# Kernel tuning notes

Measured on AMD Instinct MI355X. Metric: run time of the kernel, lower is better.

Reference implementation:

```python
import jax, jax.numpy as jnp
import numpy as np

B, N, L, OUT = 64, 100, 32, 3
EDGE_SIZES = [64, 64]   # edge MLP widths per mp step
NODE_SIZES = [64, 32]   # node MLP widths per mp step
ALPHA = 0.1             # leaky relu slope
NUM_MPS = 2
EPS = 1e-12             # for differentiable euclidean norm


def _lin_init(key, fan_in, fan_out):
    k1, k2 = jax.random.split(key)
    s = 1.0 / np.sqrt(fan_in)
    w = jax.random.uniform(k1, (fan_in, fan_out), jnp.float32, -s, s)
    b = jax.random.uniform(k2, (fan_out,), jnp.float32, -s, s)
    return w, b


def setup_inputs() -> dict:
    key = jax.random.key(0)
    ks = iter(jax.random.split(key, 32))
    inp = {"x": jax.random.normal(next(ks), (B, L), jnp.float32)}
    # global latent map: Linear(L, N*L)
    inp["lin_w"], inp["lin_b"] = _lin_init(next(ks), L, N * L)
    d = L
    for i in range(NUM_MPS):
        e_in = 2 * d + 1  # [x_i, x_j, dist_ij]
        inp[f"e{i}_w0"], inp[f"e{i}_b0"] = _lin_init(next(ks), e_in, EDGE_SIZES[0])
        inp[f"e{i}_w1"], inp[f"e{i}_b1"] = _lin_init(next(ks), EDGE_SIZES[0], EDGE_SIZES[1])
        n_in = d + EDGE_SIZES[1]  # [x, aggregated edges]
        inp[f"n{i}_w0"], inp[f"n{i}_b0"] = _lin_init(next(ks), n_in, NODE_SIZES[0])
        inp[f"n{i}_w1"], inp[f"n{i}_b1"] = _lin_init(next(ks), NODE_SIZES[0], NODE_SIZES[1])
        d = NODE_SIZES[1]
    inp["out_w"], inp["out_b"] = _lin_init(next(ks), d, OUT)
    return inp


def _mlp(h, layers, alpha):
    for w, b in layers:
        h = jax.nn.leaky_relu(h @ w + b, alpha)
    return h


def _forward(x, lin_w, lin_b,
             e0_w0, e0_b0, e0_w1, e0_b1, n0_w0, n0_b0, n0_w1, n0_b1,
             e1_w0, e1_b0, e1_w1, e1_b1, n1_w0, n1_b0, n1_w1, n1_b1,
             out_w, out_b):
    # latent map: [B, L] -> [B, N, L]
    h = (x @ lin_w + lin_b).reshape(-1, N, L)
    steps = [
        ([(e0_w0, e0_b0), (e0_w1, e0_b1)], [(n0_w0, n0_b0), (n0_w1, n0_b1)]),
        ([(e1_w0, e1_b0), (e1_w1, e1_b1)], [(n1_w0, n1_b0), (n1_w1, n1_b1)]),
    ]
    for edge_layers, node_layers in steps:
        b, n, d = h.shape
        xi = h[:, :, None, :]  # [B, N, 1, d] (receiver)
        xj = h[:, None, :, :]  # [B, 1, N, d] (sender)
        # euclidean pairwise distance, eps for differentiability at 0
        dist = jnp.sqrt(jnp.sum((xi - xj) ** 2, axis=-1, keepdims=True) + EPS)
        e_in = jnp.concatenate([
            jnp.broadcast_to(xi, (b, n, n, d)),
            jnp.broadcast_to(xj, (b, n, n, d)),
            dist,
        ], axis=-1)                       # [B, N, N, 2d+1]
        A = _mlp(e_in, edge_layers, ALPHA)  # [B, N, N, e_out]
        agg = A.sum(axis=2)               # sum over senders -> [B, N, e_out]
        h = _mlp(jnp.concatenate([h, agg], axis=-1), node_layers, ALPHA)
    out = h @ out_w + out_b               # [B, N, OUT]
    return jnp.tanh(out)                  # normalize_output=True


def reference(x, lin_w, lin_b,
              e0_w0, e0_b0, e0_w1, e0_b1, n0_w0, n0_b0, n0_w1, n0_b1,
              e1_w0, e1_b0, e1_w1, e1_b1, n1_w0, n1_b0, n1_w1, n1_b1,
              out_w, out_b):
    return _forward(x, lin_w, lin_b,
                    e0_w0, e0_b0, e0_w1, e0_b1, n0_w0, n0_b0, n0_w1, n0_b1,
                    e1_w0, e1_b0, e1_w1, e1_b1, n1_w0, n1_b0, n1_w1, n1_b1,
                    out_w, out_b)
```

## Files before the change

kernel.cpp:

```cpp
#include <hip/hip_runtime.h>

#define NB 64
#define NN 100
#define DL 32
#define BN (NB * NN)

typedef _Float16 f16x8 __attribute__((ext_vector_type(8)));
typedef float f32x4 __attribute__((ext_vector_type(4)));

static __device__ __forceinline__ float lrelu(float x) { return fmaxf(x, 0.1f * x); }
static __device__ __forceinline__ f32x4 ld4(const float* p) { return *(const f32x4*)p; }
static __device__ __forceinline__ float hsum4(f32x4 v) { return v[0] + v[1] + v[2] + v[3]; }

__global__ __launch_bounds__(256) void k_pre(
    const float* __restrict__ x, const float* __restrict__ lw, const float* __restrict__ lb,
    const float* __restrict__ ew0, const float* __restrict__ eb0,
    const float* __restrict__ w1a, const float* __restrict__ w1b,
    float* __restrict__ h, float* __restrict__ U, _Float16* __restrict__ V,
    _Float16* __restrict__ PW) {
    int blk = blockIdx.x;
    int t = threadIdx.x;
    if (blk >= 1600) {
        int step = blk - 1600;
        const float* w1 = step ? w1b : w1a;
        _Float16* dst = PW + step * 4096;
#pragma unroll
        for (int u = 0; u < 16; ++u) {
            int idx = t * 16 + u;
            int jj = idx & 7, lane = (idx >> 3) & 63, hf = (idx >> 9) & 1, kt = idx >> 10;
            int c = hf * 32 + (lane >> 4) * 8 + jj;
            int k = kt * 16 + (lane & 15);
            dst[idx] = (_Float16)w1[c * 64 + k];
        }
        return;
    }
    __shared__ float xs[DL];
    __shared__ float hs[4][DL];
    int row0 = blk * 4;
    int b = row0 / NN;
    if (t < DL) xs[t] = x[b * DL + t];
    __syncthreads();
    if (t < 128) {
        int ni = t >> 5, c = t & 31;
        int n = (row0 + ni) % NN;
        float s = lb[n * DL + c];
#pragma unroll
        for (int cc = 0; cc < DL; ++cc) s += xs[cc] * lw[cc * 3200 + n * DL + c];
        hs[ni][c] = s;
        h[(row0 + ni) * DL + c] = s;
    }
    __syncthreads();
#pragma unroll
    for (int r = 0; r < 2; ++r) {
        int o = r * 256 + t;
        int ni = o >> 7, kw = o & 127;
        int which = kw >> 6, k = kw & 63;
        const float* wp = ew0 + (which ? DL * 64 : 0) + k;
        float s = which ? 0.f : eb0[k];
#pragma unroll
        for (int c = 0; c < DL; ++c) s += hs[ni][c] * wp[c * 64];
        if (which) V[(row0 + ni) * 64 + k] = (_Float16)s;
        else       U[(row0 + ni) * 64 + k] = s;
    }
}

template <int FINAL>
__global__ __launch_bounds__(256) void k_edge(
    const float* __restrict__ h, const float* __restrict__ U, const _Float16* __restrict__ V,
    const float* __restrict__ w0, const _Float16* __restrict__ PW,
    const float* __restrict__ b1,
    const float* __restrict__ w0n, const float* __restrict__ b0n,
    const float* __restrict__ w1n, const float* __restrict__ b1n,
    const float* __restrict__ wA, const float* __restrict__ bA,
    float* __restrict__ hout, float* __restrict__ Uo, _Float16* __restrict__ Vo,
    float* __restrict__ out) {
    __shared__ __align__(16) _Float16 pwl[4096];
    __shared__ float sdist[4][112];
    __shared__ __align__(16) float sxin[4][96];
    __shared__ __align__(16) float st0[4][64];
    __shared__ __align__(16) float sh2[4][32];

    int t = threadIdx.x;
    {
        const f16x8* srcp = (const f16x8*)PW;
        f16x8* dstp = (f16x8*)pwl;
        dstp[t] = srcp[t];
        dstp[t + 256] = srcp[t + 256];
    }
    int w = t >> 6, lane = t & 63, q = lane >> 4, kk = lane & 15;
    int bi = blockIdx.x * 4 + w;
    int b = bi / NN;

    if (lane < 32) sxin[w][lane] = h[bi * DL + lane];

    {
        int g = lane >> 3, r = lane & 7;
        f32x4 hi4 = ld4(h + bi * DL + r * 4);
        const float* hb = h + b * NN * DL;
#pragma unroll
        for (int it = 0; it < 14; ++it) {
            int j = it * 8 + g;
            int jc = j < NN ? j : NN - 1;
            f32x4 hj4 = ld4(hb + jc * DL + r * 4);
            f32x4 dd = hi4 - hj4;
            float s = dd[0] * dd[0] + dd[1] * dd[1] + dd[2] * dd[2] + dd[3] * dd[3];
            s += __shfl_xor(s, 1);
            s += __shfl_xor(s, 2);
            s += __shfl_xor(s, 4);
            if (r == 0) sdist[w][j] = sqrtf(s + 1e-12f);
        }
    }

    int c0 = q * 8;
    f16x8 ulo, uhi, wdlo, wdhi;
    {
        const float* Up = U + (size_t)bi * 64;
        f32x4 a0 = ld4(Up + c0), a1 = ld4(Up + c0 + 4);
        f32x4 a2 = ld4(Up + 32 + c0), a3 = ld4(Up + 36 + c0);
        const float* wd = w0 + 64 * 64;
        f32x4 d0 = ld4(wd + c0), d1 = ld4(wd + c0 + 4);
        f32x4 d2 = ld4(wd + 32 + c0), d3 = ld4(wd + 36 + c0);
#pragma unroll
        for (int i = 0; i < 4; ++i) {
            ulo[i] = (_Float16)a0[i];  ulo[i + 4] = (_Float16)a1[i];
            uhi[i] = (_Float16)a2[i];  uhi[i + 4] = (_Float16)a3[i];
            wdlo[i] = (_Float16)d0[i]; wdlo[i + 4] = (_Float16)d1[i];
            wdhi[i] = (_Float16)d2[i]; wdhi[i + 4] = (_Float16)d3[i];
        }
    }
    float b1k[4];
#pragma unroll
    for (int kt = 0; kt < 4; ++kt) b1k[kt] = b1[kt * 16 + kk];
    float m6 = (q == 0) ? 1.f : 0.f;

    const _Float16* Vb = V + (size_t)b * NN * 64;
    f16x8 vlo, vhi;
    {
        const _Float16* vr = Vb + kk * 64 + c0;
        vlo = *(const f16x8*)vr;
        vhi = *(const f16x8*)(vr + 32);
    }

    __syncthreads();
    float dj = sdist[w][kk];

    float sacc[4] = {0.f, 0.f, 0.f, 0.f};
    unsigned pb = 0;
#pragma unroll
    for (int jt = 0; jt < 7; ++jt) {
        _Float16 djh = (_Float16)dj;
        f16x8 dj8;
#pragma unroll
        for (int i = 0; i < 8; ++i) dj8[i] = djh;
        f16x8 A0 = __builtin_elementwise_fma(dj8, wdlo, ulo + vlo);
        f16x8 A1 = __builtin_elementwise_fma(dj8, wdhi, uhi + vhi);
        A0 = __builtin_elementwise_max(A0, (_Float16)0.1f * A0);
        A1 = __builtin_elementwise_max(A1, (_Float16)0.1f * A1);

        if (jt < 6) {
            int j = (jt + 1) * 16 + kk;
            int jc = (jt == 5 && j >= NN) ? NN - 1 : j;
            const _Float16* vr = Vb + jc * 64 + c0;
            vlo = *(const f16x8*)vr;
            vhi = *(const f16x8*)(vr + 32);
            dj = sdist[w][j];
        }
        asm volatile("" : "+v"(pb));
        const _Float16* pB = (const _Float16*)((const char*)pwl + pb);
#pragma unroll
        for (int kt = 0; kt < 4; ++kt) {
            f16x8 B0 = *(const f16x8*)&pB[(kt * 2 + 0) * 512 + lane * 8];
            f16x8 B1 = *(const f16x8*)&pB[(kt * 2 + 1) * 512 + lane * 8];
            f32x4 a = {0.f, 0.f, 0.f, 0.f};
            a = __builtin_amdgcn_mfma_f32_16x16x32_f16(A0, B0, a, 0, 0, 0);
            a = __builtin_amdgcn_mfma_f32_16x16x32_f16(A1, B1, a, 0, 0, 0);
            f32x4 s4 = a + b1k[kt];
            s4 = __builtin_elementwise_max(s4, 0.1f * s4);
            float hs = hsum4(s4);
            sacc[kt] += (jt == 6) ? hs * m6 : hs;
        }
    }

    {
        float ag[4];
#pragma unroll
        for (int kt = 0; kt < 4; ++kt) {
            float s = sacc[kt];
            s += __shfl_xor(s, 16);
            s += __shfl_xor(s, 32);
            ag[kt] = s;
        }
        if (lane < 16) {
#pragma unroll
            for (int kt = 0; kt < 4; ++kt) sxin[w][32 + kt * 16 + lane] = ag[kt];
        }
    }

    {
        float sa = 0.f, sb = 0.f, sc = 0.f, sd = 0.f;
#pragma unroll
        for (int c = 0; c < 96; c += 4) {
            sa += sxin[w][c + 0] * w0n[(c + 0) * 64 + lane];
            sb += sxin[w][c + 1] * w0n[(c + 1) * 64 + lane];
            sc += sxin[w][c + 2] * w0n[(c + 2) * 64 + lane];
            sd += sxin[w][c + 3] * w0n[(c + 3) * 64 + lane];
        }
        st0[w][lane] = lrelu((sa + sb) + (sc + sd) + b0n[lane]);
    }
    {
        int k2 = lane & 31, p = lane >> 5;
        float sa = 0.f, sb = 0.f;
#pragma unroll
        for (int cc = 0; cc < 32; cc += 2) {
            int c = p * 32 + cc;
            sa += st0[w][c] * w1n[c * DL + k2];
            sb += st0[w][c + 1] * w1n[(c + 1) * DL + k2];
        }
        float s = sa + sb;
        s += __shfl_xor(s, 32);
        if (lane < 32) {
            float hv = lrelu(s + b1n[lane]);
            sh2[w][lane] = hv;
            if (!FINAL) hout[bi * DL + lane] = hv;
        }
    }

    if (FINAL) {
        if (lane < 3) {
            float s = bA[lane];
#pragma unroll
            for (int c = 0; c < DL; ++c) s += sh2[w][c] * wA[c * 3 + lane];
            out[bi * 3 + lane] = tanhf(s);
        }
    } else {
        float su = bA[lane], sv = 0.f;
#pragma unroll
        for (int c = 0; c < DL; ++c) {
            float hv = sh2[w][c];
            su += hv * wA[c * 64 + lane];
            sv += hv * wA[(DL + c) * 64 + lane];
        }
        Uo[bi * 64 + lane] = su;
        Vo[bi * 64 + lane] = (_Float16)sv;
    }
}

extern "C" void kernel_launch(void* const* d_in, const int* in_sizes, int n_in,
                              void* d_out, int out_size, void* d_ws, size_t ws_size,
                              hipStream_t stream) {
    const float* x     = (const float*)d_in[0];
    const float* lin_w = (const float*)d_in[1];
    const float* lin_b = (const float*)d_in[2];
    const float* ew0[2] = {(const float*)d_in[3],  (const float*)d_in[11]};
    const float* eb0[2] = {(const float*)d_in[4],  (const float*)d_in[12]};
    const float* ew1[2] = {(const float*)d_in[5],  (const float*)d_in[13]};
    const float* eb1[2] = {(const float*)d_in[6],  (const float*)d_in[14]};
    const float* nw0[2] = {(const float*)d_in[7],  (const float*)d_in[15]};
    const float* nb0[2] = {(const float*)d_in[8],  (const float*)d_in[16]};
    const float* nw1[2] = {(const float*)d_in[9],  (const float*)d_in[17]};
    const float* nb1[2] = {(const float*)d_in[10], (const float*)d_in[18]};
    const float* ow = (const float*)d_in[19];
    const float* ob = (const float*)d_in[20];
    float* out = (float*)d_out;

    float* h    = (float*)d_ws;
    float* h2   = h + 204800;
    float* U    = h2 + 204800;
    float* U2   = U + 409600;
    _Float16* V  = (_Float16*)(U2 + 409600);
    _Float16* V2 = V + 409600;
    _Float16* PW = V2 + 409600;

    k_pre<<<1602, 256, 0, stream>>>(x, lin_w, lin_b, ew0[0], eb0[0], ew1[0], ew1[1],
                                    h, U, V, PW);
    k_edge<0><<<1600, 256, 0, stream>>>(h, U, V, ew0[0], PW, eb1[0],
                                        nw0[0], nb0[0], nw1[0], nb1[0],
                                        ew0[1], eb0[1], h2, U2, V2, nullptr);
    k_edge<1><<<1600, 256, 0, stream>>>(h2, U2, V2, ew0[1], PW + 4096, eb1[1],
                                        nw0[1], nb0[1], nw1[1], nb1[1],
                                        ow, ob, nullptr, nullptr, nullptr, out);
}
```

Measured before the change: 174.1 us.

## Split each node's sender tiles across two waves per block

Each block now processes one receiver node with two waves that split the seven sender tiles, combining partial aggregates via shared memory. The node MLP and next-step U/V projections are also split between the two waves. This shortens the per-wave serial chain and raises parallelism. In exchange it adds block barriers and copies the shared edge weight tile into LDS once per node instead of once per four nodes.

```diff
diff --git a/kernel.cpp b/kernel.cpp
--- a/kernel.cpp
+++ b/kernel.cpp
@@ -65,7 +65,7 @@
 }
 
 template <int FINAL>
-__global__ __launch_bounds__(256) void k_edge(
+__global__ __launch_bounds__(128) void k_edge(
     const float* __restrict__ h, const float* __restrict__ U, const _Float16* __restrict__ V,
     const float* __restrict__ w0, const _Float16* __restrict__ PW,
     const float* __restrict__ b1,
@@ -75,31 +75,36 @@
     float* __restrict__ hout, float* __restrict__ Uo, _Float16* __restrict__ Vo,
     float* __restrict__ out) {
     __shared__ __align__(16) _Float16 pwl[4096];
-    __shared__ float sdist[4][112];
-    __shared__ __align__(16) float sxin[4][96];
-    __shared__ __align__(16) float st0[4][64];
-    __shared__ __align__(16) float sh2[4][32];
+    __shared__ float sdist[112];
+    __shared__ __align__(16) float sxin[32];
+    __shared__ __align__(16) float aggp[2][64];
+    __shared__ __align__(16) float red[2][64];
+    __shared__ __align__(16) float st0[64];
+    __shared__ __align__(16) float sh2[32];
 
     int t = threadIdx.x;
     {
         const f16x8* srcp = (const f16x8*)PW;
         f16x8* dstp = (f16x8*)pwl;
         dstp[t] = srcp[t];
+        dstp[t + 128] = srcp[t + 128];
         dstp[t + 256] = srcp[t + 256];
+        dstp[t + 384] = srcp[t + 384];
     }
     int w = t >> 6, lane = t & 63, q = lane >> 4, kk = lane & 15;
-    int bi = blockIdx.x * 4 + w;
+    int bi = blockIdx.x;
     int b = bi / NN;
 
-    if (lane < 32) sxin[w][lane] = h[bi * DL + lane];
+    if (t < 32) sxin[t] = h[bi * DL + t];
 
     {
         int g = lane >> 3, r = lane & 7;
+        int jbase = w * 48;
         f32x4 hi4 = ld4(h + bi * DL + r * 4);
         const float* hb = h + b * NN * DL;
 #pragma unroll
-        for (int it = 0; it < 14; ++it) {
-            int j = it * 8 + g;
+        for (int it = 0; it < 8; ++it) {
+            int j = jbase + it * 8 + g;
             int jc = j < NN ? j : NN - 1;
             f32x4 hj4 = ld4(hb + jc * DL + r * 4);
             f32x4 dd = hi4 - hj4;
@@ -107,7 +112,7 @@
             s += __shfl_xor(s, 1);
             s += __shfl_xor(s, 2);
             s += __shfl_xor(s, 4);
-            if (r == 0) sdist[w][j] = sqrtf(s + 1e-12f);
+            if (r == 0) sdist[j] = sqrtf(s + 1e-12f);
         }
     }
 
@@ -134,20 +139,21 @@
     float m6 = (q == 0) ? 1.f : 0.f;
 
     const _Float16* Vb = V + (size_t)b * NN * 64;
+    int jt0 = w ? 3 : 0;
     f16x8 vlo, vhi;
     {
-        const _Float16* vr = Vb + kk * 64 + c0;
+        const _Float16* vr = Vb + (jt0 * 16 + kk) * 64 + c0;
         vlo = *(const f16x8*)vr;
         vhi = *(const f16x8*)(vr + 32);
     }
 
     __syncthreads();
-    float dj = sdist[w][kk];
+    float dj = sdist[jt0 * 16 + kk];
 
     float sacc[4] = {0.f, 0.f, 0.f, 0.f};
     unsigned pb = 0;
-#pragma unroll
-    for (int jt = 0; jt < 7; ++jt) {
+
+    auto tile = [&](int jt, int last, int pf) {
         _Float16 djh = (_Float16)dj;
         f16x8 dj8;
 #pragma unroll
@@ -156,14 +162,13 @@
         f16x8 A1 = __builtin_elementwise_fma(dj8, wdhi, uhi + vhi);
         A0 = __builtin_elementwise_max(A0, (_Float16)0.1f * A0);
         A1 = __builtin_elementwise_max(A1, (_Float16)0.1f * A1);
-
-        if (jt < 6) {
+        if (pf) {
             int j = (jt + 1) * 16 + kk;
-            int jc = (jt == 5 && j >= NN) ? NN - 1 : j;
+            int jc = j < NN ? j : NN - 1;
             const _Float16* vr = Vb + jc * 64 + c0;
             vlo = *(const f16x8*)vr;
             vhi = *(const f16x8*)(vr + 32);
-            dj = sdist[w][j];
+            dj = sdist[j];
         }
         asm volatile("" : "+v"(pb));
         const _Float16* pB = (const _Float16*)((const char*)pwl + pb);
@@ -177,71 +182,70 @@
             f32x4 s4 = a + b1k[kt];
             s4 = __builtin_elementwise_max(s4, 0.1f * s4);
             float hs = hsum4(s4);
-            sacc[kt] += (jt == 6) ? hs * m6 : hs;
-        }
-    }
-
-    {
-        float ag[4];
+            sacc[kt] += last ? hs * m6 : hs;
+        }
+    };
+    if (w == 0) { tile(0, 0, 1); tile(1, 0, 1); tile(2, 0, 0); }
+    else        { tile(3, 0, 1); tile(4, 0, 1); tile(5, 0, 1); tile(6, 1, 0); }
+
+    {
 #pragma unroll
         for (int kt = 0; kt < 4; ++kt) {
             float s = sacc[kt];
             s += __shfl_xor(s, 16);
             s += __shfl_xor(s, 32);
-            ag[kt] = s;
-        }
-        if (lane < 16) {
-#pragma unroll
-            for (int kt = 0; kt < 4; ++kt) sxin[w][32 + kt * 16 + lane] = ag[kt];
-        }
-    }
-
-    {
-        float sa = 0.f, sb = 0.f, sc = 0.f, sd = 0.f;
-#pragma unroll
-        for (int c = 0; c < 96; c += 4) {
-            sa += sxin[w][c + 0] * w0n[(c + 0) * 64 + lane];
-            sb += sxin[w][c + 1] * w0n[(c + 1) * 64 + lane];
-            sc += sxin[w][c + 2] * w0n[(c + 2) * 64 + lane];
-            sd += sxin[w][c + 3] * w0n[(c + 3) * 64 + lane];
-        }
-        st0[w][lane] = lrelu((sa + sb) + (sc + sd) + b0n[lane]);
-    }
-    {
+            if (lane < 16) aggp[w][kt * 16 + lane] = s;
+        }
+    }
+    __syncthreads();
+
+    {
+        int k = t & 63, p = t >> 6;
+        float sa = 0.f, sb = 0.f;
+#pragma unroll
+        for (int ii = 0; ii < 48; ii += 2) {
+            int c = p * 48 + ii;
+            float x0 = (c < 32) ? sxin[c] : (aggp[0][c - 32] + aggp[1][c - 32]);
+            float x1 = (c + 1 < 32) ? sxin[c + 1] : (aggp[0][c - 31] + aggp[1][c - 31]);
+            sa += x0 * w0n[c * 64 + k];
+            sb += x1 * w0n[(c + 1) * 64 + k];
+        }
+        red[p][k] = sa + sb;
+    }
+    __syncthreads();
+    if (t < 64) st0[t] = lrelu(b0n[t] + red[0][t] + red[1][t]);
+    if (t < 64) {
         int k2 = lane & 31, p = lane >> 5;
         float sa = 0.f, sb = 0.f;
 #pragma unroll
         for (int cc = 0; cc < 32; cc += 2) {
             int c = p * 32 + cc;
-            sa += st0[w][c] * w1n[c * DL + k2];
-            sb += st0[w][c + 1] * w1n[(c + 1) * DL + k2];
+            sa += st0[c] * w1n[c * DL + k2];
+            sb += st0[c + 1] * w1n[(c + 1) * DL + k2];
         }
         float s = sa + sb;
         s += __shfl_xor(s, 32);
         if (lane < 32) {
             float hv = lrelu(s + b1n[lane]);
-            sh2[w][lane] = hv;
+            sh2[lane] = hv;
             if (!FINAL) hout[bi * DL + lane] = hv;
         }
     }
 
     if (FINAL) {
-        if (lane < 3) {
-            float s = bA[lane];
-#pragma unroll
-            for (int c = 0; c < DL; ++c) s += sh2[w][c] * wA[c * 3 + lane];
-            out[bi * 3 + lane] = tanhf(s);
+        if (t < 3) {
+            float s = bA[t];
+#pragma unroll
+            for (int c = 0; c < DL; ++c) s += sh2[c] * wA[c * 3 + t];
+            out[bi * 3 + t] = tanhf(s);
         }
     } else {
-        float su = bA[lane], sv = 0.f;
-#pragma unroll
-        for (int c = 0; c < DL; ++c) {
-            float hv = sh2[w][c];
-            su += hv * wA[c * 64 + lane];
-            sv += hv * wA[(DL + c) * 64 + lane];
-        }
-        Uo[bi * 64 + lane] = su;
-        Vo[bi * 64 + lane] = (_Float16)sv;
+        __syncthreads();
+        float s = w ? 0.f : bA[lane];
+#pragma unroll
+        for (int c = 0; c < DL; ++c) s += sh2[c] * wA[(w * DL + c) * 64 + lane];
+        if (w) Vo[bi * 64 + lane] = (_Float16)s;
+        else   Uo[bi * 64 + lane] = s;
     }
 }
 
@@ -273,10 +277,10 @@
 
     k_pre<<<1602, 256, 0, stream>>>(x, lin_w, lin_b, ew0[0], eb0[0], ew1[0], ew1[1],
                                     h, U, V, PW);
-    k_edge<0><<<1600, 256, 0, stream>>>(h, U, V, ew0[0], PW, eb1[0],
-                                        nw0[0], nb0[0], nw1[0], nb1[0],
-                                        ew0[1], eb0[1], h2, U2, V2, nullptr);
-    k_edge<1><<<1600, 256, 0, stream>>>(h2, U2, V2, ew0[1], PW + 4096, eb1[1],
-                                        nw0[1], nb0[1], nw1[1], nb1[1],
-                                        ow, ob, nullptr, nullptr, nullptr, out);
+    k_edge<0><<<BN, 128, 0, stream>>>(h, U, V, ew0[0], PW, eb1[0],
+                                      nw0[0], nb0[0], nw1[0], nb1[0],
+                                      ew0[1], eb0[1], h2, U2, V2, nullptr);
+    k_edge<1><<<BN, 128, 0, stream>>>(h2, U2, V2, ew0[1], PW + 4096, eb1[1],
+                                      nw0[1], nb0[1], nw1[1], nb1[1],
+                                      ow, ob, nullptr, nullptr, nullptr, out);
 }
```

Result: slower. 203.8 us (+17.0%).
